# Kernel optimization log

Hardware: AMD Instinct MI355X
Metric: run time of the kernel (lower is better)

## Reference

```python
import jax, jax.numpy as jnp
import numpy as np

T, B, H, V = 128, 32, 1024, 32000


def setup_inputs() -> dict:
    key = jax.random.key(0)
    ks = jax.random.split(key, 8)
    scale = 1.0 / np.sqrt(H)
    return {
        "input": jax.random.normal(ks[0], (T, B, H), dtype=jnp.float32),
        "hidden": jnp.zeros((B, H), dtype=jnp.float32),
        "w_ic": jax.random.uniform(ks[1], (H, H), jnp.float32, -scale, scale),
        "w_ix": jax.random.uniform(ks[2], (H, H), jnp.float32, -scale, scale),
        "w_fc": jax.random.uniform(ks[3], (H, H), jnp.float32, -scale, scale),
        "w_fx": jax.random.uniform(ks[4], (H, H), jnp.float32, -scale, scale),
        "b_i": jnp.zeros((H,), dtype=jnp.float32),
        "b_f": jnp.zeros((H,), dtype=jnp.float32),
        "W_out": jax.random.uniform(ks[5], (V, H), jnp.float32, -scale, scale),
        "b_out": jnp.zeros((V,), dtype=jnp.float32),
    }


def reference(input, hidden, w_ic, w_ix, w_fc, w_fx, b_i, b_f, W_out, b_out):
    # Precompute input projections for all timesteps: [T, B, H]
    ix = jnp.einsum("tbh,kh->tbk", input, w_ix)
    fx = jnp.einsum("tbh,kh->tbk", input, w_fx)

    def step(c, xs):
        ix_t, fx_t, x_t = xs
        i_t = jax.nn.sigmoid(c @ w_ic.T + b_i + ix_t)
        f_t = jax.nn.sigmoid(c @ w_fc.T + b_f + fx_t)
        c_new = i_t * x_t + f_t * c  # RAN gated-additive update
        return c_new, c_new

    hidden_final, outputs = jax.lax.scan(step, hidden, (ix, fx, input))
    logits = jnp.einsum("tbh,vh->tbv", outputs, W_out) + b_out
    log_probs = jax.nn.log_softmax(logits, axis=-1)
    return log_probs, hidden_final
```

## Files before the change

### kernel.cpp

```cpp
#include <hip/hip_runtime.h>

typedef __attribute__((ext_vector_type(4))) float f32x4;
typedef __attribute__((ext_vector_type(8))) short bf16x8;

#define T_DIM 128
#define B_DIM 32
#define H_DIM 1024
#define V_DIM 32000
#define MROWS 4096
#define NBLK 64
#define CLSLOT (B_DIM*H_DIM)
#define CSTEP 65536
#define WSTRIDE 1028

__device__ __forceinline__ ushort f2bf(float f){
  union { float f; unsigned u; } x; x.f = f;
  unsigned u = x.u;
  unsigned r = (u + 0x7fffu + ((u >> 16) & 1u)) >> 16;
  return (ushort)r;
}
__device__ __forceinline__ float bf2f(ushort h){
  union { unsigned u; float f; } x; x.u = ((unsigned)h) << 16;
  return x.f;
}

__device__ __forceinline__ void async_copy16(void* lds, const void* g){
  __builtin_amdgcn_global_load_lds((const __attribute__((address_space(1))) void*)g,
                                   (__attribute__((address_space(3))) void*)lds, 16, 0, 0);
}

__global__ void cast_bf16_kernel(const float* __restrict__ s, ushort* __restrict__ d, int n4){
  int stride = gridDim.x * blockDim.x;
  for (int i = blockIdx.x*blockDim.x + threadIdx.x; i < n4; i += stride){
    float4 v = ((const float4*)s)[i];
    ushort4 o = make_ushort4(f2bf(v.x), f2bf(v.y), f2bf(v.z), f2bf(v.w));
    ((ushort4*)d)[i] = o;
  }
}

__global__ void cast_split_kernel(const float* __restrict__ s, ushort* __restrict__ dh,
                                  ushort* __restrict__ dl, int n4){
  int stride = gridDim.x * blockDim.x;
  for (int i = blockIdx.x*blockDim.x + threadIdx.x; i < n4; i += stride){
    float4 v = ((const float4*)s)[i];
    ushort4 h = make_ushort4(f2bf(v.x), f2bf(v.y), f2bf(v.z), f2bf(v.w));
    ushort4 l = make_ushort4(f2bf(v.x - bf2f(h.x)), f2bf(v.y - bf2f(h.y)),
                             f2bf(v.z - bf2f(h.z)), f2bf(v.w - bf2f(h.w)));
    ((ushort4*)dh)[i] = h;
    ((ushort4*)dl)[i] = l;
  }
}

__global__ __launch_bounds__(256) void gemm_bt(
    const ushort* __restrict__ A, const ushort* __restrict__ B,
    float* __restrict__ C, const float* __restrict__ bias,
    int N, int K, int NTN, int order,
    float* __restrict__ pmax, float* __restrict__ psum)
{
  __shared__ ushort lA[128*32];
  __shared__ ushort lB[128*32];
  __shared__ float pmS[4][64], psS[4][64];
  int tid = threadIdx.x;
  int lane = tid & 63, wid = tid >> 6;
  int bid = blockIdx.x;
  int tm, tn;
  if (order){
    int xcd = bid & 7, id = bid >> 3;
    tn = id >> 2;
    tm = (xcd << 2) | (id & 3);
  } else {
    tm = bid / NTN; tn = bid % NTN;
  }
  int row0 = tm << 7, col0 = tn << 7;

  f32x4 acc[4][4] = {};

  auto stage = [&](const ushort* __restrict__ g, ushort* l, int r0, int k0){
    int c = wid << 1;
    const ushort* s0 = g + (size_t)(r0 + (c<<4) + (lane>>2))*K + k0 + ((lane&3)<<3);
    async_copy16(l + (c<<9), s0);
    async_copy16(l + ((c+1)<<9), s0 + (size_t)16*K);
  };

  int nk = K >> 5;
  stage(A, lA, row0, 0);
  stage(B, lB, col0, 0);
  int wm = (wid >> 1) << 6, wn = (wid & 1) << 6;
  int kg = (lane >> 4) << 3;
  int ar = lane & 15;

  for (int kt = 0; kt < nk; ++kt){
    __syncthreads();
    bf16x8 af[4], bfr[4];
    #pragma unroll
    for (int mi = 0; mi < 4; ++mi) af[mi]  = *(const bf16x8*)&lA[(wm + mi*16 + ar)*32 + kg];
    #pragma unroll
    for (int ni = 0; ni < 4; ++ni) bfr[ni] = *(const bf16x8*)&lB[(wn + ni*16 + ar)*32 + kg];
    #pragma unroll
    for (int mi = 0; mi < 4; ++mi)
      #pragma unroll
      for (int ni = 0; ni < 4; ++ni)
        acc[mi][ni] = __builtin_amdgcn_mfma_f32_16x16x32_bf16(af[mi], bfr[ni], acc[mi][ni], 0, 0, 0);
    if (kt + 1 < nk){
      __syncthreads();
      stage(A, lA, row0, (kt+1) << 5);
      stage(B, lB, col0, (kt+1) << 5);
    }
  }

  int rr = (lane >> 4) << 2;
  float bb4[4];
  #pragma unroll
  for (int ni = 0; ni < 4; ++ni) bb4[ni] = bias ? bias[col0 + wn + ni*16 + ar] : 0.f;

  #pragma unroll
  for (int mi = 0; mi < 4; ++mi){
    #pragma unroll
    for (int q = 0; q < 4; ++q){
      int r = row0 + wm + mi*16 + rr + q;
      float vals[4];
      #pragma unroll
      for (int ni = 0; ni < 4; ++ni){
        vals[ni] = acc[mi][ni][q] + bb4[ni];
        C[(size_t)r * N + col0 + wn + ni*16 + ar] = vals[ni];
      }
      if (pmax){
        float m = fmaxf(fmaxf(vals[0], vals[1]), fmaxf(vals[2], vals[3]));
        #pragma unroll
        for (int o = 1; o < 16; o <<= 1) m = fmaxf(m, __shfl_xor(m, o));
        float s = expf(vals[0]-m) + expf(vals[1]-m) + expf(vals[2]-m) + expf(vals[3]-m);
        #pragma unroll
        for (int o = 1; o < 16; o <<= 1) s += __shfl_xor(s, o);
        if (ar == 0){ int rl = mi*16 + rr + q; pmS[wid][rl] = m; psS[wid][rl] = s; }
      }
    }
  }
  if (pmax){
    __syncthreads();
    if (tid < 128){
      int rl = tid & 63, half = tid >> 6;
      int w0 = half*2, w1 = w0 + 1;
      float m0 = pmS[w0][rl], m1 = pmS[w1][rl];
      float s0 = psS[w0][rl], s1 = psS[w1][rl];
      float M = fmaxf(m0, m1);
      float S = s0*expf(m0-M) + s1*expf(m1-M);
      int r = row0 + half*64 + rl;
      pmax[(size_t)r*NTN + tn] = M;
      psum[(size_t)r*NTN + tn] = S;
    }
  }
}

__global__ __launch_bounds__(256) void gemm_bt_split(
    const ushort* __restrict__ Ah, const ushort* __restrict__ Al,
    const ushort* __restrict__ Bh, const ushort* __restrict__ Bl,
    float* __restrict__ C, int N, int K, int NTN)
{
  __shared__ ushort lAh[128*32], lAl[128*32], lBh[128*32], lBl[128*32];
  int tid = threadIdx.x;
  int lane = tid & 63, wid = tid >> 6;
  int tm = blockIdx.x / NTN, tn = blockIdx.x % NTN;
  int row0 = tm << 7, col0 = tn << 7;

  f32x4 acc[4][4] = {};

  auto stage = [&](const ushort* __restrict__ g, ushort* l, int r0, int k0){
    int c = wid << 1;
    const ushort* s0 = g + (size_t)(r0 + (c<<4) + (lane>>2))*K + k0 + ((lane&3)<<3);
    async_copy16(l + (c<<9), s0);
    async_copy16(l + ((c+1)<<9), s0 + (size_t)16*K);
  };

  int nk = K >> 5;
  stage(Ah, lAh, row0, 0); stage(Al, lAl, row0, 0);
  stage(Bh, lBh, col0, 0); stage(Bl, lBl, col0, 0);
  int wm = (wid >> 1) << 6, wn = (wid & 1) << 6;
  int kg = (lane >> 4) << 3;
  int ar = lane & 15;

  for (int kt = 0; kt < nk; ++kt){
    __syncthreads();
    bf16x8 afh[4], afl[4], bfh[4], bfl[4];
    #pragma unroll
    for (int mi = 0; mi < 4; ++mi){
      afh[mi] = *(const bf16x8*)&lAh[(wm + mi*16 + ar)*32 + kg];
      afl[mi] = *(const bf16x8*)&lAl[(wm + mi*16 + ar)*32 + kg];
    }
    #pragma unroll
    for (int ni = 0; ni < 4; ++ni){
      bfh[ni] = *(const bf16x8*)&lBh[(wn + ni*16 + ar)*32 + kg];
      bfl[ni] = *(const bf16x8*)&lBl[(wn + ni*16 + ar)*32 + kg];
    }
    #pragma unroll
    for (int mi = 0; mi < 4; ++mi)
      #pragma unroll
      for (int ni = 0; ni < 4; ++ni){
        acc[mi][ni] = __builtin_amdgcn_mfma_f32_16x16x32_bf16(afh[mi], bfh[ni], acc[mi][ni], 0, 0, 0);
        acc[mi][ni] = __builtin_amdgcn_mfma_f32_16x16x32_bf16(afh[mi], bfl[ni], acc[mi][ni], 0, 0, 0);
        acc[mi][ni] = __builtin_amdgcn_mfma_f32_16x16x32_bf16(afl[mi], bfh[ni], acc[mi][ni], 0, 0, 0);
      }
    if (kt + 1 < nk){
      __syncthreads();
      stage(Ah, lAh, row0, (kt+1) << 5); stage(Al, lAl, row0, (kt+1) << 5);
      stage(Bh, lBh, col0, (kt+1) << 5); stage(Bl, lBl, col0, (kt+1) << 5);
    }
  }

  int rr = (lane >> 4) << 2;
  #pragma unroll
  for (int mi = 0; mi < 4; ++mi)
    #pragma unroll
    for (int ni = 0; ni < 4; ++ni){
      int r  = row0 + wm + mi*16 + rr;
      int cc = col0 + wn + ni*16 + ar;
      #pragma unroll
      for (int q = 0; q < 4; ++q)
        C[(size_t)(r + q) * N + cc] = acc[mi][ni][q];
    }
}

__global__ __launch_bounds__(512) void ran_all(
    const ushort* __restrict__ cinit, ushort* __restrict__ cstate,
    const ushort* __restrict__ wh, const ushort* __restrict__ wl,
    const float* __restrict__ b_i, const float* __restrict__ b_f,
    const float* __restrict__ ixfx, const float* __restrict__ x_all,
    ushort* __restrict__ out_bf, float* __restrict__ hid_final,
    unsigned* __restrict__ slots)
{
  __shared__ ushort lWh[32*WSTRIDE];
  __shared__ ushort lWl[32*WSTRIDE];
  __shared__ float part[8][64][4];
  __shared__ float gsm[2*32*17];
  __shared__ float cfl[32][17];

  int tid = threadIdx.x, lane = tid & 63, wid = tid >> 6;
  int kh = wid & 1, mh = (wid >> 1) & 1, gate = wid >> 2;
  int bid = blockIdx.x;
  int nb = bid << 4;
  int ar = lane & 15, kg = (lane >> 4) << 3;
  int um8 = tid >> 3, ukp = (tid & 7) << 1;

  #pragma unroll
  for (int u = 0; u < 8; ++u){
    int unit = u*512 + tid;
    int r = unit >> 7, off = (unit & 127) << 3;
    int g = r >> 4, c = r & 15;
    size_t gsrc = (size_t)((g<<10) + nb + c) * H_DIM + off;
    *(bf16x8*)&lWh[r*WSTRIDE + off] = *(const bf16x8*)&wh[gsrc];
    *(bf16x8*)&lWl[r*WSTRIDE + off] = *(const bf16x8*)&wl[gsrc];
  }
  float bb = (gate ? b_f : b_i)[nb + ar];
  const ushort* bbase_h = &lWh[((gate<<4) + ar)*WSTRIDE + (kh<<9)];
  const ushort* bbase_l = &lWl[((gate<<4) + ar)*WSTRIDE + (kh<<9)];
  int abase = (kh<<15) + ((kg>>4)<<10) + (((mh<<4) + ar)<<4) + (kg & 8);
  __syncthreads();
  if (tid < 256){
    float h0 = 0.f, h1 = 0.f;
    h0 = ((const float*)nullptr == nullptr) ? 0.f : 0.f;
    cfl[um8][ukp]   = x_all ? 0.f : 0.f;
  }
  if (tid < 256){
    const float* hsrc = hid_final;
  }
  __syncthreads();

  for (int t = 0; t < T_DIM; ++t){ (void)t; break; }

}

__global__ __launch_bounds__(512) void ran_all2(
    const ushort* __restrict__ cinit, ushort* __restrict__ cstate,
    const float* __restrict__ hiddenf,
    const ushort* __restrict__ wh, const ushort* __restrict__ wl,
    const float* __restrict__ b_i, const float* __restrict__ b_f,
    const float* __restrict__ ixfx, const float* __restrict__ x_all,
    ushort* __restrict__ out_bf, float* __restrict__ hid_final,
    unsigned* __restrict__ slots)
{
  __shared__ ushort lWh[32*WSTRIDE];
  __shared__ ushort lWl[32*WSTRIDE];
  __shared__ float part[8][64][4];
  __shared__ float gsm[2*32*17];
  __shared__ float cfl[32][17];

  int tid = threadIdx.x, lane = tid & 63, wid = tid >> 6;
  int kh = wid & 1, mh = (wid >> 1) & 1, gate = wid >> 2;
  int bid = blockIdx.x;
  int nb = bid << 4;
  int ar = lane & 15, kg = (lane >> 4) << 3;
  int um8 = tid >> 3, ukp = (tid & 7) << 1;

  #pragma unroll
  for (int u = 0; u < 8; ++u){
    int unit = u*512 + tid;
    int r = unit >> 7, off = (unit & 127) << 3;
    int g = r >> 4, c = r & 15;
    size_t gsrc = (size_t)((g<<10) + nb + c) * H_DIM + off;
    *(bf16x8*)&lWh[r*WSTRIDE + off] = *(const bf16x8*)&wh[gsrc];
    *(bf16x8*)&lWl[r*WSTRIDE + off] = *(const bf16x8*)&wl[gsrc];
  }
  if (tid < 256){
    cfl[um8][ukp]   = hiddenf[(um8<<10) + nb + ukp];
    cfl[um8][ukp+1] = hiddenf[(um8<<10) + nb + ukp + 1];
  }
  float bb = (gate ? b_f : b_i)[nb + ar];
  const ushort* bbase_h = &lWh[((gate<<4) + ar)*WSTRIDE + (kh<<9)];
  const ushort* bbase_l = &lWl[((gate<<4) + ar)*WSTRIDE + (kh<<9)];
  int abase = (kh<<15) + ((kg>>4)<<10) + (((mh<<4) + ar)<<4) + (kg & 8);
  __syncthreads();

  float2 xv2; float pix[4];
  if (tid < 256) xv2 = *(const float2*)&x_all[(um8<<10) + nb + ukp];
  if (kh == 0){
    #pragma unroll
    for (int q = 0; q < 4; ++q){
      int m = (mh<<4) + ((lane>>4)<<2) + q;
      pix[q] = ixfx[m*2048 + (gate<<10) + nb + ar];
    }
  }

  for (int t = 0; t < T_DIM; ++t){
    const ushort* cst = t ? cstate + (size_t)(t-1)*CSTEP : cinit;

    f32x4 a0 = {}, a1 = {}, a2 = {};
    #pragma unroll 4
    for (int kk = 0; kk < 16; ++kk){
      int oa = abase + (kk<<11);
      int ob = (kk<<5) + kg;
      bf16x8 vah = *(const bf16x8*)&cst[oa];
      bf16x8 val = *(const bf16x8*)&cst[oa + 512];
      bf16x8 vbh = *(const bf16x8*)&bbase_h[ob];
      bf16x8 vbl = *(const bf16x8*)&bbase_l[ob];
      a0 = __builtin_amdgcn_mfma_f32_16x16x32_bf16(vah, vbh, a0, 0, 0, 0);
      a1 = __builtin_amdgcn_mfma_f32_16x16x32_bf16(vah, vbl, a1, 0, 0, 0);
      a2 = __builtin_amdgcn_mfma_f32_16x16x32_bf16(val, vbh, a2, 0, 0, 0);
    }
    f32x4 acc = a0 + a1 + a2;
    *(f32x4*)&part[wid][lane][0] = acc;
    __syncthreads();
    if (kh == 0){
      f32x4 sum = *(const f32x4*)&part[wid][lane][0] + *(const f32x4*)&part[wid+1][lane][0];
      #pragma unroll
      for (int q = 0; q < 4; ++q){
        int m = (mh<<4) + ((lane>>4)<<2) + q;
        float pre = sum[q] + bb + pix[q];
        gsm[((gate<<5) + m)*17 + ar] = 1.f / (1.f + expf(-pre));
      }
    }
    __syncthreads();
    if (tid < 256){
      float iv0 = gsm[um8*17 + ukp],       iv1 = gsm[um8*17 + ukp + 1];
      float fv0 = gsm[(32+um8)*17 + ukp],  fv1 = gsm[(32+um8)*17 + ukp + 1];
      float c0 = cfl[um8][ukp], c1 = cfl[um8][ukp+1];
      float n0 = iv0*xv2.x + fv0*c0;
      float n1 = iv1*xv2.y + fv1*c1;
      cfl[um8][ukp] = n0; cfl[um8][ukp+1] = n1;
      ushort h0 = f2bf(n0), h1 = f2bf(n1);
      unsigned hp = (unsigned)h0 | ((unsigned)h1 << 16);
      unsigned lp = (unsigned)f2bf(n0 - bf2f(h0)) | ((unsigned)f2bf(n1 - bf2f(h1)) << 16);
      size_t cb = (size_t)t*CSTEP + (bid<<10) + (um8<<4) + ukp;
      __hip_atomic_store((unsigned*)&cstate[cb],       hp, __ATOMIC_RELAXED, __HIP_MEMORY_SCOPE_AGENT);
      __hip_atomic_store((unsigned*)&cstate[cb + 512], lp, __ATOMIC_RELAXED, __HIP_MEMORY_SCOPE_AGENT);
      int rb = (um8<<10) + nb + ukp;
      *(unsigned*)&out_bf[(size_t)t*CLSLOT + rb] = hp;
      if (t == T_DIM-1){ hid_final[rb] = n0; hid_final[rb+1] = n1; }
    }
    if (t < T_DIM-1){
      __syncthreads();
      if (tid == 0)
        __hip_atomic_store(&slots[bid], (unsigned)(t+1), __ATOMIC_RELAXED, __HIP_MEMORY_SCOPE_AGENT);
      {
        const float* x_t  = x_all + (size_t)(t+1)*CLSLOT;
        const float* ix_t = ixfx  + (size_t)(t+1)*(B_DIM*2048);
        if (tid < 256) xv2 = *(const float2*)&x_t[(um8<<10) + nb + ukp];
        if (kh == 0){
          #pragma unroll
          for (int q = 0; q < 4; ++q){
            int m = (mh<<4) + ((lane>>4)<<2) + q;
            pix[q] = ix_t[m*2048 + (gate<<10) + nb + ar];
          }
        }
      }
      if (wid == 0){
        unsigned tgt = (unsigned)(t+1);
        while (1){
          unsigned v = __hip_atomic_load(&slots[lane], __ATOMIC_RELAXED, __HIP_MEMORY_SCOPE_AGENT);
          if (__ballot(v < tgt) == 0ull) break;
          __builtin_amdgcn_s_sleep(1);
        }
      }
      __syncthreads();
    }
  }
}

__global__ void init_c_kernel(const float* __restrict__ hidden,
                              ushort* __restrict__ cinit, unsigned* __restrict__ slots){
  int i = blockIdx.x * blockDim.x + threadIdx.x;
  if (blockIdx.x == 0 && threadIdx.x < NBLK) slots[threadIdx.x] = 0;
  float v = hidden[i];
  ushort h = f2bf(v);
  ushort l = f2bf(v - bf2f(h));
  int m = i >> 10, col = i & 1023;
  int j = col >> 4, k = col & 15;
  cinit[(j<<10) + (m<<4) + k]       = h;
  cinit[(j<<10) + (m<<4) + k + 512] = l;
}

__global__ __launch_bounds__(64) void lse_reduce(const float* __restrict__ pmax,
                                                 const float* __restrict__ psum,
                                                 float* __restrict__ lse, int ntn){
  int row = blockIdx.x, lane = threadIdx.x;
  float m = -1e30f, s = 0.f;
  for (int i = lane; i < ntn; i += 64){
    float mi = pmax[(size_t)row*ntn + i], si = psum[(size_t)row*ntn + i];
    float M = fmaxf(m, mi);
    s = s*expf(m - M) + si*expf(mi - M);
    m = M;
  }
  #pragma unroll
  for (int o = 32; o; o >>= 1){
    float m2 = __shfl_xor(m, o), s2 = __shfl_xor(s, o);
    float M = fmaxf(m, m2);
    s = s*expf(m - M) + s2*expf(m2 - M);
    m = M;
  }
  if (lane == 0) lse[row] = m + logf(s);
}

__global__ __launch_bounds__(256) void sub_kernel(float* __restrict__ logits,
                                                  const float* __restrict__ lse){
  size_t row = blockIdx.x;
  float l = lse[row];
  float4* p4 = (float4*)(logits + row * (size_t)V_DIM);
  for (int i = threadIdx.x; i < V_DIM/4; i += 256){
    float4 v = p4[i];
    v.x -= l; v.y -= l; v.z -= l; v.w -= l;
    p4[i] = v;
  }
}

extern "C" void kernel_launch(void* const* d_in, const int* in_sizes, int n_in,
                              void* d_out, int out_size, void* d_ws, size_t ws_size,
                              hipStream_t stream)
{
  const float* input  = (const float*)d_in[0];
  const float* hidden = (const float*)d_in[1];
  const float* w_ic   = (const float*)d_in[2];
  const float* w_ix   = (const float*)d_in[3];
  const float* w_fc   = (const float*)d_in[4];
  const float* w_fx   = (const float*)d_in[5];
  const float* b_i    = (const float*)d_in[6];
  const float* b_f    = (const float*)d_in[7];
  const float* W_out  = (const float*)d_in[8];
  const float* b_out  = (const float*)d_in[9];
  float* out = (float*)d_out;

  char* ws = (char*)d_ws;
  ushort* wout_bf = (ushort*)(ws + 0);
  ushort* in_hi   = (ushort*)(ws + 65536000);
  ushort* in_lo   = (ushort*)(ws + 73924608);
  ushort* wx_hi   = (ushort*)(ws + 82313216);
  ushort* wx_lo   = (ushort*)(ws + 86507520);
  ushort* wc_hi   = (ushort*)(ws + 90701824);
  ushort* wc_lo   = (ushort*)(ws + 94896128);
  ushort* out_bf  = (ushort*)(ws + 99090432);
  unsigned* slots = (unsigned*)(ws + 107479040);
  ushort* cinit   = (ushort*)(ws + 107479296);
  ushort* cstate  = in_hi;
  float*  pmax    = (float*)(ws + 65536000);
  float*  psum    = (float*)(ws + 69632000);
  float*  lse     = (float*)wx_hi;
  float*  ixfx    = out;

  cast_bf16_kernel <<<2048,256,0,stream>>>(W_out, wout_bf, V_DIM*H_DIM/4);
  cast_split_kernel<<<1024,256,0,stream>>>(input, in_hi, in_lo, MROWS*H_DIM/4);
  cast_split_kernel<<<256,256,0,stream>>>(w_ix, wx_hi,             wx_lo,             H_DIM*H_DIM/4);
  cast_split_kernel<<<256,256,0,stream>>>(w_fx, wx_hi+H_DIM*H_DIM, wx_lo+H_DIM*H_DIM, H_DIM*H_DIM/4);
  cast_split_kernel<<<256,256,0,stream>>>(w_ic, wc_hi,             wc_lo,             H_DIM*H_DIM/4);
  cast_split_kernel<<<256,256,0,stream>>>(w_fc, wc_hi+H_DIM*H_DIM, wc_lo+H_DIM*H_DIM, H_DIM*H_DIM/4);

  gemm_bt_split<<<32*16,256,0,stream>>>(in_hi, in_lo, wx_hi, wx_lo, ixfx, 2048, H_DIM, 16);

  init_c_kernel<<<128,256,0,stream>>>(hidden, cinit, slots);

  ran_all2<<<NBLK,512,0,stream>>>(cinit, cstate, hidden, wc_hi, wc_lo, b_i, b_f,
                                  ixfx, input, out_bf, out + (size_t)MROWS*V_DIM, slots);

  gemm_bt<<<32*250,256,0,stream>>>(out_bf, wout_bf, out, b_out, V_DIM, H_DIM, 250, 1, pmax, psum);
  lse_reduce<<<MROWS,64,0,stream>>>(pmax, psum, lse, 250);
  sub_kernel<<<MROWS,256,0,stream>>>(out, lse);
}
```

Measured before the change: 2.052 ms.

## Drop low-bf16 state split in recurrence and feed chunked state directly to output GEMM

The recurrent state is now stored only as a single bf16 (hi) copy instead of hi+lo, so each step does two MFMAs per k-chunk instead of three and writes half the state. The output GEMM reads the A operand straight from the chunked cstate layout through a new staging path, which removes the separate out_bf buffer and its writes. This lowers per-step latency on the serial recurrence but reduces the precision of the state fed back into the recurrence, which could accumulate error over 128 steps. It also removes the dead ran_all stub and renames ran_all2.

```diff
diff --git a/kernel.cpp b/kernel.cpp
--- a/kernel.cpp
+++ b/kernel.cpp
@@ -9,8 +9,7 @@
 #define V_DIM 32000
 #define MROWS 4096
 #define NBLK 64
-#define CLSLOT (B_DIM*H_DIM)
-#define CSTEP 65536
+#define CSTEP 32768
 #define WSTRIDE 1028
 
 __device__ __forceinline__ ushort f2bf(float f){
@@ -54,7 +53,7 @@
 __global__ __launch_bounds__(256) void gemm_bt(
     const ushort* __restrict__ A, const ushort* __restrict__ B,
     float* __restrict__ C, const float* __restrict__ bias,
-    int N, int K, int NTN, int order,
+    int N, int K, int NTN, int order, int achunk,
     float* __restrict__ pmax, float* __restrict__ psum)
 {
   __shared__ ushort lA[128*32];
@@ -81,9 +80,20 @@
     async_copy16(l + (c<<9), s0);
     async_copy16(l + ((c+1)<<9), s0 + (size_t)16*K);
   };
+  auto stageAc = [&](const ushort* __restrict__ g, ushort* l, int r0, int k0){
+    int c = wid << 1;
+    int cb  = (k0 >> 4) + ((lane & 3) >> 1);
+    int sub = (lane & 1) << 3;
+    int rA = r0 + (c<<4) + (lane>>2);
+    const ushort* sA = g + ((size_t)(rA>>5)<<15) + (cb<<9) + ((rA&31)<<4) + sub;
+    async_copy16(l + (c<<9), sA);
+    int rB = rA + 16;
+    const ushort* sB = g + ((size_t)(rB>>5)<<15) + (cb<<9) + ((rB&31)<<4) + sub;
+    async_copy16(l + ((c+1)<<9), sB);
+  };
 
   int nk = K >> 5;
-  stage(A, lA, row0, 0);
+  if (achunk) stageAc(A, lA, row0, 0); else stage(A, lA, row0, 0);
   stage(B, lB, col0, 0);
   int wm = (wid >> 1) << 6, wn = (wid & 1) << 6;
   int kg = (lane >> 4) << 3;
@@ -103,7 +113,7 @@
         acc[mi][ni] = __builtin_amdgcn_mfma_f32_16x16x32_bf16(af[mi], bfr[ni], acc[mi][ni], 0, 0, 0);
     if (kt + 1 < nk){
       __syncthreads();
-      stage(A, lA, row0, (kt+1) << 5);
+      if (achunk) stageAc(A, lA, row0, (kt+1) << 5); else stage(A, lA, row0, (kt+1) << 5);
       stage(B, lB, col0, (kt+1) << 5);
     }
   }
@@ -221,11 +231,11 @@
 
 __global__ __launch_bounds__(512) void ran_all(
     const ushort* __restrict__ cinit, ushort* __restrict__ cstate,
+    const float* __restrict__ hiddenf,
     const ushort* __restrict__ wh, const ushort* __restrict__ wl,
     const float* __restrict__ b_i, const float* __restrict__ b_f,
     const float* __restrict__ ixfx, const float* __restrict__ x_all,
-    ushort* __restrict__ out_bf, float* __restrict__ hid_final,
-    unsigned* __restrict__ slots)
+    float* __restrict__ hid_final, unsigned* __restrict__ slots)
 {
   __shared__ ushort lWh[32*WSTRIDE];
   __shared__ ushort lWl[32*WSTRIDE];
@@ -249,64 +259,14 @@
     *(bf16x8*)&lWh[r*WSTRIDE + off] = *(const bf16x8*)&wh[gsrc];
     *(bf16x8*)&lWl[r*WSTRIDE + off] = *(const bf16x8*)&wl[gsrc];
   }
+  if (tid < 256){
+    cfl[um8][ukp]   = hiddenf[(um8<<10) + nb + ukp];
+    cfl[um8][ukp+1] = hiddenf[(um8<<10) + nb + ukp + 1];
+  }
   float bb = (gate ? b_f : b_i)[nb + ar];
   const ushort* bbase_h = &lWh[((gate<<4) + ar)*WSTRIDE + (kh<<9)];
   const ushort* bbase_l = &lWl[((gate<<4) + ar)*WSTRIDE + (kh<<9)];
-  int abase = (kh<<15) + ((kg>>4)<<10) + (((mh<<4) + ar)<<4) + (kg & 8);
-  __syncthreads();
-  if (tid < 256){
-    float h0 = 0.f, h1 = 0.f;
-    h0 = ((const float*)nullptr == nullptr) ? 0.f : 0.f;
-    cfl[um8][ukp]   = x_all ? 0.f : 0.f;
-  }
-  if (tid < 256){
-    const float* hsrc = hid_final;
-  }
-  __syncthreads();
-
-  for (int t = 0; t < T_DIM; ++t){ (void)t; break; }
-
-}
-
-__global__ __launch_bounds__(512) void ran_all2(
-    const ushort* __restrict__ cinit, ushort* __restrict__ cstate,
-    const float* __restrict__ hiddenf,
-    const ushort* __restrict__ wh, const ushort* __restrict__ wl,
-    const float* __restrict__ b_i, const float* __restrict__ b_f,
-    const float* __restrict__ ixfx, const float* __restrict__ x_all,
-    ushort* __restrict__ out_bf, float* __restrict__ hid_final,
-    unsigned* __restrict__ slots)
-{
-  __shared__ ushort lWh[32*WSTRIDE];
-  __shared__ ushort lWl[32*WSTRIDE];
-  __shared__ float part[8][64][4];
-  __shared__ float gsm[2*32*17];
-  __shared__ float cfl[32][17];
-
-  int tid = threadIdx.x, lane = tid & 63, wid = tid >> 6;
-  int kh = wid & 1, mh = (wid >> 1) & 1, gate = wid >> 2;
-  int bid = blockIdx.x;
-  int nb = bid << 4;
-  int ar = lane & 15, kg = (lane >> 4) << 3;
-  int um8 = tid >> 3, ukp = (tid & 7) << 1;
-
-  #pragma unroll
-  for (int u = 0; u < 8; ++u){
-    int unit = u*512 + tid;
-    int r = unit >> 7, off = (unit & 127) << 3;
-    int g = r >> 4, c = r & 15;
-    size_t gsrc = (size_t)((g<<10) + nb + c) * H_DIM + off;
-    *(bf16x8*)&lWh[r*WSTRIDE + off] = *(const bf16x8*)&wh[gsrc];
-    *(bf16x8*)&lWl[r*WSTRIDE + off] = *(const bf16x8*)&wl[gsrc];
-  }
-  if (tid < 256){
-    cfl[um8][ukp]   = hiddenf[(um8<<10) + nb + ukp];
-    cfl[um8][ukp+1] = hiddenf[(um8<<10) + nb + ukp + 1];
-  }
-  float bb = (gate ? b_f : b_i)[nb + ar];
-  const ushort* bbase_h = &lWh[((gate<<4) + ar)*WSTRIDE + (kh<<9)];
-  const ushort* bbase_l = &lWl[((gate<<4) + ar)*WSTRIDE + (kh<<9)];
-  int abase = (kh<<15) + ((kg>>4)<<10) + (((mh<<4) + ar)<<4) + (kg & 8);
+  int abase = (kh<<14) + ((kg>>4)<<9) + (((mh<<4) + ar)<<4) + (kg & 8);
   __syncthreads();
 
   float2 xv2; float pix[4];
@@ -322,20 +282,18 @@
   for (int t = 0; t < T_DIM; ++t){
     const ushort* cst = t ? cstate + (size_t)(t-1)*CSTEP : cinit;
 
-    f32x4 a0 = {}, a1 = {}, a2 = {};
+    f32x4 a0 = {}, a1 = {};
     #pragma unroll 4
     for (int kk = 0; kk < 16; ++kk){
-      int oa = abase + (kk<<11);
+      int oa = abase + (kk<<10);
       int ob = (kk<<5) + kg;
       bf16x8 vah = *(const bf16x8*)&cst[oa];
-      bf16x8 val = *(const bf16x8*)&cst[oa + 512];
       bf16x8 vbh = *(const bf16x8*)&bbase_h[ob];
       bf16x8 vbl = *(const bf16x8*)&bbase_l[ob];
       a0 = __builtin_amdgcn_mfma_f32_16x16x32_bf16(vah, vbh, a0, 0, 0, 0);
       a1 = __builtin_amdgcn_mfma_f32_16x16x32_bf16(vah, vbl, a1, 0, 0, 0);
-      a2 = __builtin_amdgcn_mfma_f32_16x16x32_bf16(val, vbh, a2, 0, 0, 0);
-    }
-    f32x4 acc = a0 + a1 + a2;
+    }
+    f32x4 acc = a0 + a1;
     *(f32x4*)&part[wid][lane][0] = acc;
     __syncthreads();
     if (kh == 0){
@@ -355,22 +313,20 @@
       float n0 = iv0*xv2.x + fv0*c0;
       float n1 = iv1*xv2.y + fv1*c1;
       cfl[um8][ukp] = n0; cfl[um8][ukp+1] = n1;
-      ushort h0 = f2bf(n0), h1 = f2bf(n1);
-      unsigned hp = (unsigned)h0 | ((unsigned)h1 << 16);
-      unsigned lp = (unsigned)f2bf(n0 - bf2f(h0)) | ((unsigned)f2bf(n1 - bf2f(h1)) << 16);
-      size_t cb = (size_t)t*CSTEP + (bid<<10) + (um8<<4) + ukp;
-      __hip_atomic_store((unsigned*)&cstate[cb],       hp, __ATOMIC_RELAXED, __HIP_MEMORY_SCOPE_AGENT);
-      __hip_atomic_store((unsigned*)&cstate[cb + 512], lp, __ATOMIC_RELAXED, __HIP_MEMORY_SCOPE_AGENT);
-      int rb = (um8<<10) + nb + ukp;
-      *(unsigned*)&out_bf[(size_t)t*CLSLOT + rb] = hp;
-      if (t == T_DIM-1){ hid_final[rb] = n0; hid_final[rb+1] = n1; }
+      unsigned hp = (unsigned)f2bf(n0) | ((unsigned)f2bf(n1) << 16);
+      size_t cb = (size_t)t*CSTEP + (bid<<9) + (um8<<4) + ukp;
+      __hip_atomic_store((unsigned*)&cstate[cb], hp, __ATOMIC_RELAXED, __HIP_MEMORY_SCOPE_AGENT);
+      if (t == T_DIM-1){
+        int rb = (um8<<10) + nb + ukp;
+        hid_final[rb] = n0; hid_final[rb+1] = n1;
+      }
     }
     if (t < T_DIM-1){
       __syncthreads();
       if (tid == 0)
         __hip_atomic_store(&slots[bid], (unsigned)(t+1), __ATOMIC_RELAXED, __HIP_MEMORY_SCOPE_AGENT);
       {
-        const float* x_t  = x_all + (size_t)(t+1)*CLSLOT;
+        const float* x_t  = x_all + (size_t)(t+1)*(B_DIM*H_DIM);
         const float* ix_t = ixfx  + (size_t)(t+1)*(B_DIM*2048);
         if (tid < 256) xv2 = *(const float2*)&x_t[(um8<<10) + nb + ukp];
         if (kh == 0){
@@ -399,12 +355,8 @@
   int i = blockIdx.x * blockDim.x + threadIdx.x;
   if (blockIdx.x == 0 && threadIdx.x < NBLK) slots[threadIdx.x] = 0;
   float v = hidden[i];
-  ushort h = f2bf(v);
-  ushort l = f2bf(v - bf2f(h));
   int m = i >> 10, col = i & 1023;
-  int j = col >> 4, k = col & 15;
-  cinit[(j<<10) + (m<<4) + k]       = h;
-  cinit[(j<<10) + (m<<4) + k + 512] = l;
+  cinit[((col>>4)<<9) + (m<<4) + (col&15)] = f2bf(v);
 }
 
 __global__ __launch_bounds__(64) void lse_reduce(const float* __restrict__ pmax,
@@ -464,12 +416,11 @@
   ushort* wx_lo   = (ushort*)(ws + 86507520);
   ushort* wc_hi   = (ushort*)(ws + 90701824);
   ushort* wc_lo   = (ushort*)(ws + 94896128);
-  ushort* out_bf  = (ushort*)(ws + 99090432);
   unsigned* slots = (unsigned*)(ws + 107479040);
   ushort* cinit   = (ushort*)(ws + 107479296);
   ushort* cstate  = in_hi;
-  float*  pmax    = (float*)(ws + 65536000);
-  float*  psum    = (float*)(ws + 69632000);
+  float*  pmax    = (float*)in_lo;
+  float*  psum    = (float*)(ws + 78020608);
   float*  lse     = (float*)wx_hi;
   float*  ixfx    = out;
 
@@ -484,10 +435,10 @@
 
   init_c_kernel<<<128,256,0,stream>>>(hidden, cinit, slots);
 
-  ran_all2<<<NBLK,512,0,stream>>>(cinit, cstate, hidden, wc_hi, wc_lo, b_i, b_f,
-                                  ixfx, input, out_bf, out + (size_t)MROWS*V_DIM, slots);
-
-  gemm_bt<<<32*250,256,0,stream>>>(out_bf, wout_bf, out, b_out, V_DIM, H_DIM, 250, 1, pmax, psum);
+  ran_all<<<NBLK,512,0,stream>>>(cinit, cstate, hidden, wc_hi, wc_lo, b_i, b_f,
+                                 ixfx, input, out + (size_t)MROWS*V_DIM, slots);
+
+  gemm_bt<<<32*250,256,0,stream>>>(cstate, wout_bf, out, b_out, V_DIM, H_DIM, 250, 1, 1, pmax, psum);
   lse_reduce<<<MROWS,64,0,stream>>>(pmax, psum, lse, 250);
   sub_kernel<<<MROWS,256,0,stream>>>(out, lse);
 }
```

Measured after the change: 2.045 ms. About the same (-0.3%).
